# Optimization experiments

Measured on AMD Instinct MI355X. Metric: run time of the kernel, lower is better.

## Reference

```python
import jax, jax.numpy as jnp
import numpy as np

EMB = 384
HEADS = 6
HEAD_SIZE = 64


def setup_inputs() -> dict:
    key = jax.random.key(0)
    ks = jax.random.split(key, 6)
    B, T = 128, 256
    x = jax.random.normal(ks[0], (B, T, EMB), dtype=jnp.float32)
    s = EMB ** -0.5
    Wq = jax.random.normal(ks[1], (HEADS, EMB, HEAD_SIZE), dtype=jnp.float32) * s
    Wk = jax.random.normal(ks[2], (HEADS, EMB, HEAD_SIZE), dtype=jnp.float32) * s
    Wv = jax.random.normal(ks[3], (HEADS, EMB, HEAD_SIZE), dtype=jnp.float32) * s
    Wproj = jax.random.normal(ks[4], (EMB, EMB), dtype=jnp.float32) * s
    bproj = jax.random.normal(ks[5], (EMB,), dtype=jnp.float32) * 0.01
    return {"x": x, "Wq": Wq, "Wk": Wk, "Wv": Wv, "Wproj": Wproj, "bproj": bproj}


def reference(x, Wq, Wk, Wv, Wproj, bproj):
    B, T, C = x.shape
    scale = C ** -0.5  # original scales by embeddingSize**-0.5, not headSize
    q = jnp.einsum('bte,hed->bhtd', x, Wq)
    k = jnp.einsum('bte,hed->bhtd', x, Wk)
    v = jnp.einsum('bte,hed->bhtd', x, Wv)
    w = jnp.einsum('bhtd,bhsd->bhts', q, k) * scale  # (B,H,T,T)
    mask = jnp.tril(jnp.ones((T, T), dtype=bool))
    w = jnp.where(mask[None, None], w, -jnp.inf)
    # original applies softmax over dim=1 of (B,T,T) -> the query axis -> axis=2 here
    w = jax.nn.softmax(w, axis=2)
    out = jnp.einsum('bhts,bhsd->bhtd', w, v)  # (B,H,T,Dh)
    out = out.transpose(0, 2, 1, 3).reshape(B, T, -1)  # concat heads -> (B,T,EMB)
    return out @ Wproj + bproj  # dropout omitted (eval mode)
```

## Files before the change

### kernel.cpp

```cpp
#include <hip/hip_runtime.h>

#define EMB 384
#define HEADS 6
#define DH 64
#define TT 256

constexpr float SCALE = 0.05103103630798288f;

typedef __attribute__((ext_vector_type(8))) short short8;
typedef __attribute__((ext_vector_type(4))) float f32x4;
typedef __attribute__((ext_vector_type(4))) unsigned short u16x4;

__device__ __forceinline__ unsigned short f2bf(float f) {
  unsigned int u = __builtin_bit_cast(unsigned int, f);
  u += 0x7FFFu + ((u >> 16) & 1u);
  return (unsigned short)(u >> 16);
}
__device__ __forceinline__ float bf2f(unsigned short u) {
  unsigned int v = ((unsigned int)u) << 16;
  return __builtin_bit_cast(float, v);
}
__device__ __forceinline__ void gll16(const void* g, void* l) {
  __builtin_amdgcn_global_load_lds(
      (const __attribute__((address_space(1))) unsigned int*)g,
      (__attribute__((address_space(3))) unsigned int*)l, 16, 0, 0);
}

__global__ __launch_bounds__(256)
void cvt_x(const float* __restrict__ x, unsigned short* __restrict__ xb, int n8) {
  int i = blockIdx.x * 256 + threadIdx.x;
  if (i < n8) {
    const float4* src = (const float4*)x;
    float4 a = src[i * 2], b = src[i * 2 + 1];
    short8 o;
    o[0] = (short)f2bf(a.x); o[1] = (short)f2bf(a.y);
    o[2] = (short)f2bf(a.z); o[3] = (short)f2bf(a.w);
    o[4] = (short)f2bf(b.x); o[5] = (short)f2bf(b.y);
    o[6] = (short)f2bf(b.z); o[7] = (short)f2bf(b.w);
    ((short8*)xb)[i] = o;
  }
}

__global__ __launch_bounds__(256)
void build_wt(const float* __restrict__ Wq, const float* __restrict__ Wk,
              const float* __restrict__ Wv, const float* __restrict__ Wp,
              unsigned short* __restrict__ Wt) {
  int idx = blockIdx.x * 256 + threadIdx.x;
  int n = idx / 48, e0 = (idx % 48) * 8;
  const float* src; int stride;
  if (n < 1152) {
    int h = n / 192, rem = n % 192, qkv = rem >> 6, d = rem & 63;
    const float* W = (qkv == 0) ? Wq : (qkv == 1) ? Wk : Wv;
    src = W + ((size_t)h * EMB + e0) * DH + d; stride = DH;
  } else {
    int c = n - 1152;
    src = Wp + (size_t)e0 * EMB + c; stride = EMB;
  }
  short8 o;
  #pragma unroll
  for (int j = 0; j < 8; ++j) o[j] = (short)f2bf(src[j * stride]);
  ((short8*)Wt)[idx] = o;
}

__global__ __launch_bounds__(512, 1)
void qkv_attn(const unsigned short* __restrict__ xb16, const unsigned short* __restrict__ Wt,
              unsigned short* __restrict__ O)
{
  __shared__ __align__(16) char EL[73728];
  __shared__ __align__(16) char KL[32768];
  __shared__ __align__(16) char VL[32768];
  __shared__ float Lpart[8][256];
  __shared__ float invL[256];

  const int bh = blockIdx.x, tid = (int)threadIdx.x;
  const int w = tid >> 6, lane = tid & 63;
  const int la = lane & 15, kh = lane >> 4;
  const int b = bh / 6, h = bh - b * 6;
  const unsigned short* xb = xb16 + (size_t)b * 256 * 384;
  const unsigned short* Wb = Wt + (size_t)h * 192 * 384;
  char* AL = EL;
  char* BL = EL + 32768;

  const int wr = (w >> 1) * 64, wc = (w & 1) * 96;
  f32x4 acc[4][6];
  #pragma unroll
  for (int i = 0; i < 4; ++i)
    #pragma unroll
    for (int j = 0; j < 6; ++j) acc[i][j] = f32x4{0.f, 0.f, 0.f, 0.f};

  for (int kt = 0; kt < 6; ++kt) {
    if (kt) __syncthreads();
    #pragma unroll
    for (int i = 0; i < 4; ++i) {
      const int Lb = i * 8192 + tid * 16;
      const int row = Lb >> 7;
      const int kcs = ((Lb >> 4) & 7) ^ (row & 7);
      gll16(xb + (size_t)row * 384 + kt * 64 + kcs * 8, AL + Lb);
    }
    #pragma unroll
    for (int i = 0; i < 3; ++i) {
      const int Lb = i * 8192 + tid * 16;
      const int row = Lb >> 7;
      const int kcs = ((Lb >> 4) & 7) ^ (row & 7);
      gll16(Wb + (size_t)row * 384 + kt * 64 + kcs * 8, BL + Lb);
    }
    __syncthreads();
    #pragma unroll
    for (int kk = 0; kk < 2; ++kk) {
      const int ch = kk * 4 + kh;
      short8 a[4], bfr[6];
      #pragma unroll
      for (int mi = 0; mi < 4; ++mi) {
        const int r = wr + mi * 16 + la;
        a[mi] = *(const short8*)(AL + r * 128 + ((ch ^ (r & 7)) << 4));
      }
      #pragma unroll
      for (int ni = 0; ni < 6; ++ni) {
        const int rB = wc + ni * 16 + la;
        bfr[ni] = *(const short8*)(BL + rB * 128 + ((ch ^ (rB & 7)) << 4));
      }
      __builtin_amdgcn_s_setprio(1);
      #pragma unroll
      for (int mi = 0; mi < 4; ++mi)
        #pragma unroll
        for (int ni = 0; ni < 6; ++ni)
          acc[mi][ni] = __builtin_amdgcn_mfma_f32_16x16x32_bf16(a[mi], bfr[ni], acc[mi][ni], 0, 0, 0);
      __builtin_amdgcn_s_setprio(0);
    }
  }
  __syncthreads();

  #pragma unroll
  for (int mi = 0; mi < 4; ++mi) {
    #pragma unroll
    for (int ni = 0; ni < 6; ++ni) {
      const int col = wc + ni * 16 + la;
      const int tb = wr + mi * 16 + kh * 4;
      if (col < 64) {
        const int d = col;
        #pragma unroll
        for (int j = 0; j < 4; ++j) {
          const int t = tb + j;
          *(unsigned short*)(EL + t * 128 + (((d >> 3) ^ (t & 7)) << 4) + (d & 7) * 2)
              = f2bf(acc[mi][ni][j]);
        }
      } else if (col < 128) {
        const int d = col - 64;
        #pragma unroll
        for (int j = 0; j < 4; ++j) {
          const int t = tb + j;
          *(unsigned short*)(KL + t * 128 + (((d >> 3) ^ (t & 7)) << 4) + (d & 7) * 2)
              = f2bf(acc[mi][ni][j]);
        }
      } else {
        const int d = col - 128;
        u16x4 pk;
        #pragma unroll
        for (int j = 0; j < 4; ++j) pk[j] = f2bf(acc[mi][ni][j]);
        *(u16x4*)(VL + d * 512 + (((tb >> 3) ^ (d & 7)) << 4) + (tb & 7) * 2) = pk;
      }
    }
  }
  __syncthreads();

  const int rts[2] = { w, 15 - w };
  short8 qa[2][2];
  #pragma unroll
  for (int ti = 0; ti < 2; ++ti)
    #pragma unroll
    for (int kk = 0; kk < 2; ++kk) {
      const int r = rts[ti] * 16 + la;
      const int ch = kk * 4 + kh;
      qa[ti][kk] = *(const short8*)(EL + r * 128 + ((ch ^ (r & 7)) << 4));
    }
  __syncthreads();

  int wps[2], eoffs[2];
  #pragma unroll
  for (int ti = 0; ti < 2; ++ti) {
    const int rt = rts[ti];
    wps[ti] = 32 * ((rt + 2) >> 1);
    const int S = (rt & 1) ? ((rt + 1) * (rt + 1) / 4) : (rt * (rt + 2) / 4);
    eoffs[ti] = 1024 * S;
  }

  #pragma unroll
  for (int i = 0; i < 4; ++i) Lpart[w][i * 64 + lane] = 0.f;

  #pragma unroll
  for (int ti = 0; ti < 2; ++ti) {
    const int rt = rts[ti], wp = wps[ti], stride = wp * 2;
    char* Ebase = EL + eoffs[ti];
    const int nns = wp >> 4;
    for (int ns = 0; ns < nns; ++ns) {
      f32x4 s4 = f32x4{0.f, 0.f, 0.f, 0.f};
      #pragma unroll
      for (int kk = 0; kk < 2; ++kk) {
        const int rB = ns * 16 + la, kc = kk * 4 + kh;
        short8 bf = *(const short8*)(KL + rB * 128 + ((kc ^ (rB & 7)) << 4));
        s4 = __builtin_amdgcn_mfma_f32_16x16x32_bf16(qa[ti][kk], bf, s4, 0, 0, 0);
      }
      const int c = ns * 16 + la, cc = c >> 3, co = (c & 7) * 2;
      float ps = 0.f;
      #pragma unroll
      for (int j = 0; j < 4; ++j) {
        const int r = kh * 4 + j;
        const int t = rt * 16 + r;
        const float e = (t >= c) ? __expf(s4[j] * SCALE) : 0.f;
        ps += e;
        *(unsigned short*)(Ebase + r * stride + ((cc ^ (r & 3)) << 4) + co) = f2bf(e);
      }
      ps += __shfl_xor(ps, 16);
      ps += __shfl_xor(ps, 32);
      if (kh == 0) Lpart[w][c] += ps;
    }
  }
  __syncthreads();

  if (tid < 256) {
    float Ls = 0.f;
    #pragma unroll
    for (int ww = 0; ww < 8; ++ww) Ls += Lpart[ww][tid];
    invL[tid] = 1.f / Ls;
  }
  __syncthreads();

  {
    const int d = tid >> 3, qq = tid & 7;
    #pragma unroll
    for (int i = 0; i < 4; ++i) {
      const int kcp = qq * 4 + i;
      char* p = VL + d * 512 + kcp * 16;
      short8 v = *(short8*)p;
      const int sb = (kcp ^ (d & 7)) * 8;
      short8 o;
      #pragma unroll
      for (int e = 0; e < 8; ++e)
        o[e] = (short)f2bf(bf2f((unsigned short)v[e]) * invL[sb + e]);
      *(short8*)p = o;
    }
  }
  __syncthreads();

  unsigned short* Og = O + (size_t)b * 256 * 384 + h * 64;
  #pragma unroll
  for (int ti = 0; ti < 2; ++ti) {
    const int rt = rts[ti], wp = wps[ti], stride = wp * 2;
    const char* Ebase = EL + eoffs[ti];
    f32x4 oacc[4];
    #pragma unroll
    for (int nd = 0; nd < 4; ++nd) oacc[nd] = f32x4{0.f, 0.f, 0.f, 0.f};
    const int nks = wp >> 5;
    for (int ks = 0; ks < nks; ++ks) {
      const int cc = ks * 4 + kh;
      short8 ea = *(const short8*)(Ebase + la * stride + ((cc ^ (la & 3)) << 4));
      __builtin_amdgcn_s_setprio(1);
      #pragma unroll
      for (int nd = 0; nd < 4; ++nd) {
        const int d = nd * 16 + la;
        short8 vb = *(const short8*)(VL + d * 512 + ((cc ^ (d & 7)) << 4));
        oacc[nd] = __builtin_amdgcn_mfma_f32_16x16x32_bf16(ea, vb, oacc[nd], 0, 0, 0);
      }
      __builtin_amdgcn_s_setprio(0);
    }
    #pragma unroll
    for (int nd = 0; nd < 4; ++nd) {
      const int d = nd * 16 + la;
      #pragma unroll
      for (int j = 0; j < 4; ++j) {
        const int t = rt * 16 + kh * 4 + j;
        Og[(size_t)t * 384 + d] = f2bf(oacc[nd][j]);
      }
    }
  }
}

__global__ __launch_bounds__(512, 1)
void proj_gemm(const unsigned short* __restrict__ A, const unsigned short* __restrict__ Bt,
               float* __restrict__ Co, const float* __restrict__ bias)
{
  __shared__ __align__(16) unsigned short AL[128 * 384];
  __shared__ __align__(16) unsigned short BL[2][128 * 64];
  const int tid = (int)threadIdx.x, w = tid >> 6, lane = tid & 63;
  const int la = lane & 15, kh = lane >> 4;
  const int m0 = blockIdx.x * 128;

  {
    const int row = tid >> 2, qq = tid & 3;
    const short8* O8 = (const short8*)(A + (size_t)(m0 + row) * 384);
    #pragma unroll
    for (int i = 0; i < 12; ++i) {
      const int ch = qq + 4 * i;
      *(short8*)((char*)AL + row * 768 + ((ch ^ (row & 7)) << 4)) = O8[ch];
    }
  }

  auto stageB = [&](int buf, int n0, int k0) {
    #pragma unroll
    for (int i = 0; i < 2; ++i) {
      const int Lb = i * 8192 + tid * 16;
      const int row = Lb >> 7;
      const int kcs = ((Lb >> 4) & 7) ^ (row & 7);
      gll16(Bt + (size_t)(n0 + row) * 384 + k0 + kcs * 8, (char*)BL[buf] + Lb);
    }
  };

  stageB(0, 0, 0);
  __syncthreads();

  const int wr = (w >> 2) * 64, wc = (w & 3) * 32;
  int buf = 0;
  for (int nt = 0; nt < 3; ++nt) {
    f32x4 acc[4][2];
    #pragma unroll
    for (int i = 0; i < 4; ++i) { acc[i][0] = f32x4{0.f,0.f,0.f,0.f}; acc[i][1] = f32x4{0.f,0.f,0.f,0.f}; }

    for (int kt = 0; kt < 6; ++kt) {
      if (kt < 5)          stageB(buf ^ 1, nt * 128, (kt + 1) * 64);
      else if (nt + 1 < 3) stageB(buf ^ 1, (nt + 1) * 128, 0);
      #pragma unroll
      for (int kk = 0; kk < 2; ++kk) {
        short8 a[4], b[2];
        const int chA = kt * 8 + kk * 4 + kh;
        #pragma unroll
        for (int mi = 0; mi < 4; ++mi) {
          const int r = wr + mi * 16 + la;
          a[mi] = *(const short8*)((const char*)AL + r * 768 + ((chA ^ (r & 7)) << 4));
        }
        const int chB = kk * 4 + kh;
        #pragma unroll
        for (int ni = 0; ni < 2; ++ni) {
          const int rB = wc + ni * 16 + la;
          b[ni] = *(const short8*)((const char*)BL[buf] + rB * 128 + ((chB ^ (rB & 7)) << 4));
        }
        __builtin_amdgcn_s_setprio(1);
        #pragma unroll
        for (int mi = 0; mi < 4; ++mi)
          #pragma unroll
          for (int ni = 0; ni < 2; ++ni)
            acc[mi][ni] = __builtin_amdgcn_mfma_f32_16x16x32_bf16(a[mi], b[ni], acc[mi][ni], 0, 0, 0);
        __builtin_amdgcn_s_setprio(0);
      }
      __syncthreads();
      buf ^= 1;
    }

    #pragma unroll
    for (int mi = 0; mi < 4; ++mi) {
      const int mbase = m0 + wr + mi * 16 + kh * 4;
      #pragma unroll
      for (int ni = 0; ni < 2; ++ni) {
        const int nl = nt * 128 + wc + ni * 16 + la;
        const float bn = bias[nl];
        #pragma unroll
        for (int j = 0; j < 4; ++j)
          Co[(size_t)(mbase + j) * 384 + nl] = acc[mi][ni][j] + bn;
      }
    }
  }
}

__global__ __launch_bounds__(256, 1)
void mha_fused(const float* __restrict__ x, const float* __restrict__ Wq,
               const float* __restrict__ Wk, const float* __restrict__ Wv,
               const float* __restrict__ Wp, const float* __restrict__ bp,
               float* __restrict__ out)
{
  const int bh = blockIdx.x;
  const int b = bh / HEADS, h = bh % HEADS;
  const int tid = (int)threadIdx.x;
  const int wave = tid >> 6, lane = tid & 63;
  const float* xb = x + (size_t)b * TT * EMB;
  const float* wq = Wq + (size_t)h * EMB * DH;
  const float* wk = Wk + (size_t)h * EMB * DH;
  const float* wv = Wv + (size_t)h * EMB * DH;
  __shared__ float Ks[TT][68];
  __shared__ float Vs[TT][64];
  __shared__ float Qt[64][68];
  for (int c = 0; c < 4; ++c) {
    const int s0 = wave * 64 + c * 16;
    float ak[16], av[16];
    #pragma unroll
    for (int r = 0; r < 16; ++r) { ak[r] = 0.f; av[r] = 0.f; }
    for (int e = 0; e < EMB; ++e) {
      const float kk = wk[e * DH + lane];
      const float vv = wv[e * DH + lane];
      #pragma unroll
      for (int r = 0; r < 16; ++r) {
        const float xv = xb[(s0 + r) * EMB + e];
        ak[r] += xv * kk; av[r] += xv * vv;
      }
    }
    #pragma unroll
    for (int r = 0; r < 16; ++r) { Ks[s0 + r][lane] = ak[r]; Vs[s0 + r][lane] = av[r]; }
  }
  __syncthreads();
  const int s = tid;
  float kreg[64];
  {
    const float4* k4 = (const float4*)&Ks[s][0];
    #pragma unroll
    for (int i = 0; i < 16; ++i) {
      float4 kv = k4[i];
      kreg[4*i+0] = kv.x; kreg[4*i+1] = kv.y; kreg[4*i+2] = kv.z; kreg[4*i+3] = kv.w;
    }
  }
  float Lsum = 0.f;
  for (int tile = 0; tile < 4; ++tile) {
    {
      const int r0 = tile * 64 + wave * 16;
      float aq[16];
      #pragma unroll
      for (int r = 0; r < 16; ++r) aq[r] = 0.f;
      for (int e = 0; e < EMB; ++e) {
        const float qw = wq[e * DH + lane];
        #pragma unroll
        for (int r = 0; r < 16; ++r) aq[r] += xb[(r0 + r) * EMB + e] * qw;
      }
      __syncthreads();
      #pragma unroll
      for (int r = 0; r < 16; ++r) Qt[wave*16 + r][lane] = aq[r];
      __syncthreads();
    }
    const int tbase = tile * 64;
    if (tbase + 63 >= s) {
      for (int tr = 0; tr < 64; ++tr) {
        const int t = tbase + tr;
        if (t < s) continue;
        float w = 0.f;
        const float4* q4 = (const float4*)&Qt[tr][0];
        #pragma unroll
        for (int i = 0; i < 16; ++i) {
          float4 qv = q4[i];
          w += qv.x*kreg[4*i+0] + qv.y*kreg[4*i+1] + qv.z*kreg[4*i+2] + qv.w*kreg[4*i+3];
        }
        Lsum += __expf(w * SCALE);
      }
    }
  }
  __syncthreads();
  {
    const float invL = 1.0f / Lsum;
    float4* v4 = (float4*)&Vs[s][0];
    #pragma unroll
    for (int i = 0; i < 16; ++i) {
      float4 vv = v4[i];
      vv.x *= invL; vv.y *= invL; vv.z *= invL; vv.w *= invL;
      v4[i] = vv;
    }
  }
  __syncthreads();
  const float bias1 = bp[tid];
  const float bias2 = (tid < 128) ? bp[256 + tid] : 0.f;
  const int tr = tid >> 2, dq = tid & 3;
  float* ob = out + (size_t)b * TT * EMB;
  for (int tile = 0; tile < 4; ++tile) {
    {
      const int r0 = tile * 64 + wave * 16;
      float aq[16];
      #pragma unroll
      for (int r = 0; r < 16; ++r) aq[r] = 0.f;
      for (int e = 0; e < EMB; ++e) {
        const float qw = wq[e * DH + lane];
        #pragma unroll
        for (int r = 0; r < 16; ++r) aq[r] += xb[(r0 + r) * EMB + e] * qw;
      }
      __syncthreads();
      #pragma unroll
      for (int r = 0; r < 16; ++r) Qt[wave*16 + r][lane] = aq[r];
      __syncthreads();
    }
    const int t = tile * 64 + tr;
    float qreg[16];
    {
      const float4* q4 = (const float4*)&Qt[tr][dq * 16];
      #pragma unroll
      for (int i = 0; i < 4; ++i) {
        float4 qv = q4[i];
        qreg[4*i+0] = qv.x; qreg[4*i+1] = qv.y; qreg[4*i+2] = qv.z; qreg[4*i+3] = qv.w;
      }
    }
    float acc[16];
    #pragma unroll
    for (int i = 0; i < 16; ++i) acc[i] = 0.f;
    for (int s2 = 0; s2 <= t; ++s2) {
      const float4* kk4 = (const float4*)&Ks[s2][dq * 16];
      float part = 0.f;
      #pragma unroll
      for (int i = 0; i < 4; ++i) {
        float4 kv = kk4[i];
        part += qreg[4*i+0]*kv.x + qreg[4*i+1]*kv.y + qreg[4*i+2]*kv.z + qreg[4*i+3]*kv.w;
      }
      part += __shfl_xor(part, 1);
      part += __shfl_xor(part, 2);
      const float p = __expf(part * SCALE);
      const float4* vv4 = (const float4*)&Vs[s2][dq * 16];
      #pragma unroll
      for (int i = 0; i < 4; ++i) {
        float4 vv = vv4[i];
        acc[4*i+0] += p * vv.x; acc[4*i+1] += p * vv.y;
        acc[4*i+2] += p * vv.z; acc[4*i+3] += p * vv.w;
      }
    }
    __syncthreads();
    #pragma unroll
    for (int i = 0; i < 16; ++i) Qt[tr][dq*16 + i] = acc[i];
    __syncthreads();
    const int c1 = tid;
    const int c2 = 256 + tid;
    for (int rg = 0; rg < 4; ++rg) {
      float a1[16], a2[16];
      #pragma unroll
      for (int r = 0; r < 16; ++r) { a1[r] = 0.f; a2[r] = 0.f; }
      for (int d = 0; d < 64; ++d) {
        const float wp1 = Wp[(size_t)(h*64 + d) * EMB + c1];
        const float wp2 = (tid < 128) ? Wp[(size_t)(h*64 + d) * EMB + c2] : 0.f;
        #pragma unroll
        for (int r = 0; r < 16; ++r) {
          const float a = Qt[rg*16 + r][d];
          a1[r] += a * wp1; a2[r] += a * wp2;
        }
      }
      if (h == 0) {
        #pragma unroll
        for (int r = 0; r < 16; ++r) { a1[r] += bias1; a2[r] += bias2; }
      }
      const int trow0 = tile*64 + rg*16;
      #pragma unroll
      for (int r = 0; r < 16; ++r)
        atomicAdd(&ob[(size_t)(trow0 + r) * EMB + c1], a1[r]);
      if (tid < 128) {
        #pragma unroll
        for (int r = 0; r < 16; ++r)
          atomicAdd(&ob[(size_t)(trow0 + r) * EMB + c2], a2[r]);
      }
    }
    __syncthreads();
  }
}

extern "C" void kernel_launch(void* const* d_in, const int* in_sizes, int n_in,
                              void* d_out, int out_size, void* d_ws, size_t ws_size,
                              hipStream_t stream) {
  const float* x  = (const float*)d_in[0];
  const float* Wq = (const float*)d_in[1];
  const float* Wk = (const float*)d_in[2];
  const float* Wv = (const float*)d_in[3];
  const float* Wp = (const float*)d_in[4];
  const float* bp = (const float*)d_in[5];

  const int nb = in_sizes[0] / (TT * EMB);
  const size_t M = (size_t)nb * TT;
  const size_t XB = M * EMB * 2;
  const size_t WT = (size_t)1536 * 384 * 2;

  const size_t off_x  = 0;
  const size_t off_wt = XB;
  const size_t off_o  = off_wt + WT;
  const size_t need   = off_o + XB;

  if (ws_size < need) {
    hipMemsetAsync(d_out, 0, (size_t)out_size * sizeof(float), stream);
    mha_fused<<<nb * HEADS, 256, 0, stream>>>(x, Wq, Wk, Wv, Wp, bp, (float*)d_out);
    return;
  }

  char* ws = (char*)d_ws;
  unsigned short* xb16 = (unsigned short*)(ws + off_x);
  unsigned short* Wt   = (unsigned short*)(ws + off_wt);
  unsigned short* Ow   = (unsigned short*)(ws + off_o);

  const int n8 = (int)(M * EMB / 8);
  cvt_x<<<(n8 + 255) / 256, 256, 0, stream>>>(x, xb16, n8);
  build_wt<<<288, 256, 0, stream>>>(Wq, Wk, Wv, Wp, Wt);

  qkv_attn<<<nb * HEADS, 512, 0, stream>>>(xb16, Wt, Ow);

  proj_gemm<<<(unsigned)(M / 128), 512, 0, stream>>>(
      Ow, Wt + (size_t)1152 * 384, (float*)d_out, bp);
}
```

Measured before the change: 118.7 us.

## Double qkv_attn block to 1024 threads and split work across 16 waves

Raises the fused QKV+attention kernel from 512 to 1024 threads per block, shrinking each wave's QKV GEMM tile to 64x48, interleaving score column strips between wave pairs, and giving each wave of a pair one of the two row tiles in the PV stage. The aim is more waves per CU to hide latency and cut per-wave register pressure, since LDS use limits the kernel to one block per CU. In exchange there are more partial-sum rows to reduce, more barrier participants, and an uneven PV split because the two causal row tiles have different lengths.

```diff
diff --git a/kernel.cpp b/kernel.cpp
--- a/kernel.cpp
+++ b/kernel.cpp
@@ -62,14 +62,14 @@
   ((short8*)Wt)[idx] = o;
 }
 
-__global__ __launch_bounds__(512, 1)
+__global__ __launch_bounds__(1024, 1)
 void qkv_attn(const unsigned short* __restrict__ xb16, const unsigned short* __restrict__ Wt,
               unsigned short* __restrict__ O)
 {
   __shared__ __align__(16) char EL[73728];
   __shared__ __align__(16) char KL[32768];
   __shared__ __align__(16) char VL[32768];
-  __shared__ float Lpart[8][256];
+  __shared__ float Lpart[16][256];
   __shared__ float invL[256];
 
   const int bh = blockIdx.x, tid = (int)threadIdx.x;
@@ -81,41 +81,46 @@
   char* AL = EL;
   char* BL = EL + 32768;
 
-  const int wr = (w >> 1) * 64, wc = (w & 1) * 96;
-  f32x4 acc[4][6];
+  const int wr = (w >> 2) * 64, wc = (w & 3) * 48;
+  f32x4 acc[4][3];
   #pragma unroll
   for (int i = 0; i < 4; ++i)
     #pragma unroll
-    for (int j = 0; j < 6; ++j) acc[i][j] = f32x4{0.f, 0.f, 0.f, 0.f};
+    for (int j = 0; j < 3; ++j) acc[i][j] = f32x4{0.f, 0.f, 0.f, 0.f};
 
   for (int kt = 0; kt < 6; ++kt) {
     if (kt) __syncthreads();
     #pragma unroll
-    for (int i = 0; i < 4; ++i) {
-      const int Lb = i * 8192 + tid * 16;
+    for (int i = 0; i < 2; ++i) {
+      const int Lb = i * 16384 + tid * 16;
       const int row = Lb >> 7;
       const int kcs = ((Lb >> 4) & 7) ^ (row & 7);
       gll16(xb + (size_t)row * 384 + kt * 64 + kcs * 8, AL + Lb);
     }
-    #pragma unroll
-    for (int i = 0; i < 3; ++i) {
-      const int Lb = i * 8192 + tid * 16;
-      const int row = Lb >> 7;
-      const int kcs = ((Lb >> 4) & 7) ^ (row & 7);
-      gll16(Wb + (size_t)row * 384 + kt * 64 + kcs * 8, BL + Lb);
+    {
+      const int Lb0 = tid * 16;
+      const int row0 = Lb0 >> 7;
+      const int kcs0 = ((Lb0 >> 4) & 7) ^ (row0 & 7);
+      gll16(Wb + (size_t)row0 * 384 + kt * 64 + kcs0 * 8, BL + Lb0);
+      if (tid < 512) {
+        const int Lb = 16384 + tid * 16;
+        const int row = Lb >> 7;
+        const int kcs = ((Lb >> 4) & 7) ^ (row & 7);
+        gll16(Wb + (size_t)row * 384 + kt * 64 + kcs * 8, BL + Lb);
+      }
     }
     __syncthreads();
     #pragma unroll
     for (int kk = 0; kk < 2; ++kk) {
       const int ch = kk * 4 + kh;
-      short8 a[4], bfr[6];
+      short8 a[4], bfr[3];
       #pragma unroll
       for (int mi = 0; mi < 4; ++mi) {
         const int r = wr + mi * 16 + la;
         a[mi] = *(const short8*)(AL + r * 128 + ((ch ^ (r & 7)) << 4));
       }
       #pragma unroll
-      for (int ni = 0; ni < 6; ++ni) {
+      for (int ni = 0; ni < 3; ++ni) {
         const int rB = wc + ni * 16 + la;
         bfr[ni] = *(const short8*)(BL + rB * 128 + ((ch ^ (rB & 7)) << 4));
       }
@@ -123,7 +128,7 @@
       #pragma unroll
       for (int mi = 0; mi < 4; ++mi)
         #pragma unroll
-        for (int ni = 0; ni < 6; ++ni)
+        for (int ni = 0; ni < 3; ++ni)
           acc[mi][ni] = __builtin_amdgcn_mfma_f32_16x16x32_bf16(a[mi], bfr[ni], acc[mi][ni], 0, 0, 0);
       __builtin_amdgcn_s_setprio(0);
     }
@@ -133,7 +138,7 @@
   #pragma unroll
   for (int mi = 0; mi < 4; ++mi) {
     #pragma unroll
-    for (int ni = 0; ni < 6; ++ni) {
+    for (int ni = 0; ni < 3; ++ni) {
       const int col = wc + ni * 16 + la;
       const int tb = wr + mi * 16 + kh * 4;
       if (col < 64) {
@@ -163,7 +168,8 @@
   }
   __syncthreads();
 
-  const int rts[2] = { w, 15 - w };
+  const int p = w >> 1;
+  const int rts[2] = { p, 15 - p };
   short8 qa[2][2];
   #pragma unroll
   for (int ti = 0; ti < 2; ++ti)
@@ -192,7 +198,7 @@
     const int rt = rts[ti], wp = wps[ti], stride = wp * 2;
     char* Ebase = EL + eoffs[ti];
     const int nns = wp >> 4;
-    for (int ns = 0; ns < nns; ++ns) {
+    for (int ns = (w & 1); ns < nns; ns += 2) {
       f32x4 s4 = f32x4{0.f, 0.f, 0.f, 0.f};
       #pragma unroll
       for (int kk = 0; kk < 2; ++kk) {
@@ -220,31 +226,31 @@
   if (tid < 256) {
     float Ls = 0.f;
     #pragma unroll
-    for (int ww = 0; ww < 8; ++ww) Ls += Lpart[ww][tid];
+    for (int ww = 0; ww < 16; ++ww) Ls += Lpart[ww][tid];
     invL[tid] = 1.f / Ls;
   }
   __syncthreads();
 
   {
-    const int d = tid >> 3, qq = tid & 7;
-    #pragma unroll
-    for (int i = 0; i < 4; ++i) {
-      const int kcp = qq * 4 + i;
-      char* p = VL + d * 512 + kcp * 16;
-      short8 v = *(short8*)p;
+    const int d = tid >> 4, qq = tid & 15;
+    #pragma unroll
+    for (int i = 0; i < 2; ++i) {
+      const int kcp = qq * 2 + i;
+      char* pch = VL + d * 512 + kcp * 16;
+      short8 v = *(short8*)pch;
       const int sb = (kcp ^ (d & 7)) * 8;
       short8 o;
       #pragma unroll
       for (int e = 0; e < 8; ++e)
         o[e] = (short)f2bf(bf2f((unsigned short)v[e]) * invL[sb + e]);
-      *(short8*)p = o;
+      *(short8*)pch = o;
     }
   }
   __syncthreads();
 
   unsigned short* Og = O + (size_t)b * 256 * 384 + h * 64;
-  #pragma unroll
-  for (int ti = 0; ti < 2; ++ti) {
+  {
+    const int ti = (w & 1) ? 0 : 1;
     const int rt = rts[ti], wp = wps[ti], stride = wp * 2;
     const char* Ebase = EL + eoffs[ti];
     f32x4 oacc[4];
@@ -320,7 +326,7 @@
       else if (nt + 1 < 3) stageB(buf ^ 1, (nt + 1) * 128, 0);
       #pragma unroll
       for (int kk = 0; kk < 2; ++kk) {
-        short8 a[4], b[2];
+        short8 a[4], bb[2];
         const int chA = kt * 8 + kk * 4 + kh;
         #pragma unroll
         for (int mi = 0; mi < 4; ++mi) {
@@ -331,14 +337,14 @@
         #pragma unroll
         for (int ni = 0; ni < 2; ++ni) {
           const int rB = wc + ni * 16 + la;
-          b[ni] = *(const short8*)((const char*)BL[buf] + rB * 128 + ((chB ^ (rB & 7)) << 4));
+          bb[ni] = *(const short8*)((const char*)BL[buf] + rB * 128 + ((chB ^ (rB & 7)) << 4));
         }
         __builtin_amdgcn_s_setprio(1);
         #pragma unroll
         for (int mi = 0; mi < 4; ++mi)
           #pragma unroll
           for (int ni = 0; ni < 2; ++ni)
-            acc[mi][ni] = __builtin_amdgcn_mfma_f32_16x16x32_bf16(a[mi], b[ni], acc[mi][ni], 0, 0, 0);
+            acc[mi][ni] = __builtin_amdgcn_mfma_f32_16x16x32_bf16(a[mi], bb[ni], acc[mi][ni], 0, 0, 0);
         __builtin_amdgcn_s_setprio(0);
       }
       __syncthreads();
@@ -574,7 +580,7 @@
   cvt_x<<<(n8 + 255) / 256, 256, 0, stream>>>(x, xb16, n8);
   build_wt<<<288, 256, 0, stream>>>(Wq, Wk, Wv, Wp, Wt);
 
-  qkv_attn<<<nb * HEADS, 512, 0, stream>>>(xb16, Wt, Ow);
+  qkv_attn<<<nb * HEADS, 1024, 0, stream>>>(xb16, Wt, Ow);
 
   proj_gemm<<<(unsigned)(M / 128), 512, 0, stream>>>(
       Ow, Wt + (size_t)1152 * 384, (float*)d_out, bp);
```

Result: no change. 117.0 us (-1.5%).
